# Kernel optimization log

Hardware: AMD Instinct MI355X
Metric: run time of the kernel (lower is better)

## Reference

```python
import jax, jax.numpy as jnp
import numpy as np

D_MODEL, D_STATE, D_CONV, D_INNER = 1024, 16, 4, 2048
B, S = 1, 2048
EPS = 1e-5


def setup_inputs() -> dict:
    key = jax.random.key(0)
    ks = jax.random.split(key, 8)
    sc = 0.02
    return {
        "x": jax.random.normal(ks[0], (B, S, D_MODEL), jnp.float32),
        "ln_g": jnp.ones((D_MODEL,), jnp.float32),
        "ln_b": jnp.zeros((D_MODEL,), jnp.float32),
        "in_w": jax.random.normal(ks[1], (2 * D_INNER, D_MODEL), jnp.float32) * sc,
        "conv_w": jax.random.normal(ks[2], (D_INNER, 1, D_CONV), jnp.float32) * sc,  # depthwise OIH
        "conv_b": jax.random.normal(ks[3], (D_INNER,), jnp.float32) * sc,
        "xproj_w": jax.random.normal(ks[4], (2 * D_STATE + 1, D_INNER), jnp.float32) * sc,
        "dt_w": jax.random.normal(ks[5], (D_INNER, 1), jnp.float32) * sc,
        "dt_b": jax.random.normal(ks[6], (D_INNER,), jnp.float32) * sc,
        "A_log": jnp.log(jnp.arange(1, D_STATE + 1, dtype=jnp.float32)),
        "D": jnp.ones((D_INNER,), jnp.float32),
        "out_w": jax.random.normal(ks[7], (D_MODEL, D_INNER), jnp.float32) * sc,
    }


def reference(x, ln_g, ln_b, in_w, conv_w, conv_b, xproj_w, dt_w, dt_b, A_log, D, out_w):
    b, s, _ = x.shape
    d_inner = D.shape[0]
    d_state = A_log.shape[0]
    d_conv = conv_w.shape[-1]
    residual = x

    # LayerNorm
    mu = jnp.mean(x, axis=-1, keepdims=True)
    var = jnp.mean(jnp.square(x - mu), axis=-1, keepdims=True)
    xn = (x - mu) * jax.lax.rsqrt(var + EPS) * ln_g + ln_b

    # in_proj, split into x and gate z
    xz = jnp.einsum('bsd,ed->bse', xn, in_w)  # [B,S,2*d_inner]
    xi, z = jnp.split(xz, 2, axis=-1)

    # causal depthwise conv1d (torch pads d_conv-1 both sides then crops to seq_len)
    xc = jnp.transpose(xi, (0, 2, 1))  # [B,C,S]
    xc = jnp.pad(xc, ((0, 0), (0, 0), (d_conv - 1, 0)))
    xc = jax.lax.conv_general_dilated(
        xc, conv_w, window_strides=(1,), padding='VALID',
        dimension_numbers=('NCH', 'OIH', 'NCH'), feature_group_count=d_inner)
    xc = xc + conv_b[None, :, None]
    xs = jax.nn.silu(jnp.transpose(xc, (0, 2, 1)))  # [B,S,d_inner]

    # SSM projections
    xp = jnp.einsum('bsd,ed->bse', xs, xproj_w)  # [B,S,2*d_state+1]
    delta = jax.nn.softplus(xp[..., :1] * dt_w[:, 0] + dt_b)  # [B,S,d_inner]
    Bm = xp[..., 1:1 + d_state]  # [B,S,N]
    Cm = xp[..., 1 + d_state:]   # [B,S,N]
    A = -jnp.exp(A_log)          # [N]

    dA = jnp.exp(delta[..., None] * A)                      # [B,S,d_inner,N]
    dBx = delta[..., None] * Bm[:, :, None, :] * xs[..., None]  # [B,S,d_inner,N]

    def step(h, inp):
        dA_t, dBx_t, C_t = inp
        h = dA_t * h + dBx_t                     # [B,d_inner,N]
        y_t = jnp.einsum('bdn,bn->bd', h, C_t)   # [B,d_inner]
        return h, y_t

    h0 = jnp.zeros((b, d_inner, d_state), x.dtype)
    _, ys = jax.lax.scan(step, h0, (jnp.moveaxis(dA, 1, 0),
                                    jnp.moveaxis(dBx, 1, 0),
                                    jnp.moveaxis(Cm, 1, 0)))
    y = jnp.moveaxis(ys, 0, 1) + xs * D  # [B,S,d_inner]

    y = y * jax.nn.silu(z)
    out = jnp.einsum('bse,de->bsd', y, out_w)
    return out + residual
```

## Files before the change

kernel.cpp:

```cpp
#include <hip/hip_runtime.h>
#include <cstdint>
#include <cstddef>

#define D_MODEL 1024
#define D_STATE 16
#define D_CONV  4
#define D_INNER 2048
#define SEQ     2048
#define NCHUNK  128
#define CLEN    16
#define NGRP    8
#define GCH     16
#define LN_EPS  1e-5f

typedef unsigned short ushort_t;
typedef __attribute__((ext_vector_type(8))) short short8;
typedef __attribute__((ext_vector_type(4))) float f32x4;

__device__ __forceinline__ ushort_t f2bf(float x) {
  union { float f; uint32_t u; } v; v.f = x;
  uint32_t r = (v.u + 0x7fffu + ((v.u >> 16) & 1u)) >> 16;
  return (ushort_t)r;
}
__device__ __forceinline__ float bf2f(ushort_t u) {
  union { uint32_t x; float f; } v; v.x = ((uint32_t)u) << 16; return v.f;
}

__device__ __forceinline__ void async16(void* lds, const void* g) {
  __builtin_amdgcn_global_load_lds(
      (const __attribute__((address_space(1))) unsigned int*)g,
      (__attribute__((address_space(3))) unsigned int*)lds, 16, 0, 0);
}

__device__ __forceinline__ float softplus_f(float x) {
  if (x > 20.f) return x;
  if (x < -20.f) return __expf(x);
  return __logf(1.f + __expf(x));
}

__device__ __forceinline__ void dapow(float g1, float* da) {
  float g2 = g1 * g1, g4 = g2 * g2, g8 = g4 * g4;
  #pragma unroll
  for (int n = 0; n < 16; n++) {
    int e = n + 1;
    float v = (e & 1) ? g1 : 1.f;
    if (e & 2) v *= g2;
    if (e & 4) v *= g4;
    if (e & 8) v *= g8;
    da[n] = v;
  }
}

__global__ __launch_bounds__(256) void prep_kernel(const float* __restrict__ x,
                                                   const float* __restrict__ g,
                                                   const float* __restrict__ b,
                                                   const float* __restrict__ inw,
                                                   const float* __restrict__ outw,
                                                   const float* __restrict__ xpw,
                                                   ushort_t* __restrict__ xn_bf,
                                                   ushort_t* __restrict__ inw_bf,
                                                   ushort_t* __restrict__ outw_bf,
                                                   ushort_t* __restrict__ xpw_bf) {
  int blk = blockIdx.x;
  if (blk < SEQ) {
    int row = blk;
    const float4* xr = (const float4*)(x + (size_t)row * D_MODEL);
    float4 v = xr[threadIdx.x];
    float s  = v.x + v.y + v.z + v.w;
    float ss = v.x * v.x + v.y * v.y + v.z * v.z + v.w * v.w;
    #pragma unroll
    for (int o = 32; o; o >>= 1) { s += __shfl_down(s, o); ss += __shfl_down(ss, o); }
    __shared__ float sbuf[8], ssbuf[8];
    int wid = threadIdx.x >> 6, lane = threadIdx.x & 63;
    if (lane == 0) { sbuf[wid] = s; ssbuf[wid] = ss; }
    __syncthreads();
    if (threadIdx.x == 0) {
      float t = 0.f, t2 = 0.f;
      for (int i = 0; i < 4; i++) { t += sbuf[i]; t2 += ssbuf[i]; }
      float mu = t / D_MODEL;
      sbuf[4] = mu;
      ssbuf[4] = rsqrtf(t2 / D_MODEL - mu * mu + LN_EPS);
    }
    __syncthreads();
    float mu = sbuf[4], inv = ssbuf[4];
    float4 gv = ((const float4*)g)[threadIdx.x];
    float4 bv = ((const float4*)b)[threadIdx.x];
    ushort_t o4[4];
    o4[0] = f2bf((v.x - mu) * inv * gv.x + bv.x);
    o4[1] = f2bf((v.y - mu) * inv * gv.y + bv.y);
    o4[2] = f2bf((v.z - mu) * inv * gv.z + bv.z);
    o4[3] = f2bf((v.w - mu) * inv * gv.w + bv.w);
    *(ushort4*)&xn_bf[(size_t)row * D_MODEL + threadIdx.x * 4] =
        make_ushort4(o4[0], o4[1], o4[2], o4[3]);
  } else {
    int idx = (blk - SEQ) * 256 + threadIdx.x;
    const int n1 = 2 * D_INNER * D_MODEL;
    const int n2 = D_MODEL * D_INNER;
    const int n3 = 64 * D_INNER;
    if (idx < n1) {
      inw_bf[idx] = f2bf(inw[idx]);
    } else if (idx < n1 + n2) {
      int j = idx - n1;
      outw_bf[j] = f2bf(outw[j]);
    } else if (idx < n1 + n2 + n3) {
      int j = idx - n1 - n2;
      xpw_bf[j] = (j < 33 * D_INNER) ? f2bf(xpw[j]) : (ushort_t)0;
    }
  }
}

template <int BM, int BN, int KDIM, int EPI, int NBUF, int KSPLIT>
__global__ __launch_bounds__(256, 2) void gemm_pipe(const ushort_t* __restrict__ A,
                                                    const ushort_t* __restrict__ B,
                                                    void* __restrict__ Cout,
                                                    const float* __restrict__ R,
                                                    int N) {
  constexpr int KT = KDIM / 32 / KSPLIT;
  constexpr int K2 = KDIM * 2;
  constexpr int IA = BM / 64, IB = BN / 64;
  constexpr int S  = IA + IB;
  constexpr int W  = (NBUF - 2) * S;
  constexpr int WTM = BM / 2, WTN = BN / 2;
  constexpr int MREP = WTM / 16, NREP = WTN / 16;
  __shared__ __align__(16) ushort_t As[NBUF][BM * 32];
  __shared__ __align__(16) ushort_t Bs[NBUF][BN * 32];

  const int nwg = gridDim.x * gridDim.y;
  int bid = blockIdx.y * gridDim.x + blockIdx.x;
  int swz = (bid & 7) * (nwg >> 3) + (bid >> 3);
  int bn = swz % gridDim.x, bm = swz / gridDim.x;
  int ks = 0;
  if constexpr (KSPLIT > 1) { ks = bn; bn = 0; }
  const int tid = threadIdx.x, wid = tid >> 6, lane = tid & 63;
  const int wm = wid >> 1, wn = wid & 1;
  const int row0A = bm * BM, row0B = bn * BN;
  const size_t kbase = (size_t)ks * KT * 64;

  const char* gA[IA];
  const char* gB[IB];
  #pragma unroll
  for (int i = 0; i < IA; i++) {
    int o = i * 4096 + tid * 16;
    int r = o >> 6, src = (o & 63) ^ ((r & 3) << 4);
    gA[i] = (const char*)A + (size_t)(row0A + r) * K2 + src + kbase;
  }
  #pragma unroll
  for (int i = 0; i < IB; i++) {
    int o = i * 4096 + tid * 16;
    int r = o >> 6, src = (o & 63) ^ ((r & 3) << 4);
    gB[i] = (const char*)B + (size_t)(row0B + r) * K2 + src + kbase;
  }
  const int ldsW = wid * 1024;

  auto STAGE = [&](int bb, int kt) {
    int kb = kt * 64;
    #pragma unroll
    for (int i = 0; i < IA; i++)
      async16((char*)&As[bb][0] + i * 4096 + ldsW, gA[i] + kb);
    #pragma unroll
    for (int i = 0; i < IB; i++)
      async16((char*)&Bs[bb][0] + i * 4096 + ldsW, gB[i] + kb);
  };

  #pragma unroll
  for (int p = 0; p < NBUF - 1; p++) STAGE(p, p);

  int offA[MREP], offB[NREP];
  #pragma unroll
  for (int m = 0; m < MREP; m++) {
    int row = wm * WTM + m * 16 + (lane & 15);
    offA[m] = row * 64 + ((((lane >> 4)) ^ (row & 3)) << 4);
  }
  #pragma unroll
  for (int n = 0; n < NREP; n++) {
    int row = wn * WTN + n * 16 + (lane & 15);
    offB[n] = row * 64 + ((((lane >> 4)) ^ (row & 3)) << 4);
  }

  f32x4 acc[MREP][NREP] = {};
  int cur = 0;
  for (int kt = 0; kt < KT; kt++) {
    if (kt < KT - 1) {
      if constexpr (W == 6)       asm volatile("s_waitcnt vmcnt(6)" ::: "memory");
      else if constexpr (W == 8)  asm volatile("s_waitcnt vmcnt(8)" ::: "memory");
      else if constexpr (W == 12) asm volatile("s_waitcnt vmcnt(12)" ::: "memory");
      else                        asm volatile("s_waitcnt vmcnt(0)" ::: "memory");
    } else {
      asm volatile("s_waitcnt vmcnt(0)" ::: "memory");
    }
    __builtin_amdgcn_s_barrier();
    __builtin_amdgcn_sched_barrier(0);
    const char* Ab = (const char*)&As[cur][0];
    const char* Bb = (const char*)&Bs[cur][0];
    short8 af[MREP], bf[NREP];
    #pragma unroll
    for (int m = 0; m < MREP; m++) af[m] = *(const short8*)(Ab + offA[m]);
    #pragma unroll
    for (int n = 0; n < NREP; n++) bf[n] = *(const short8*)(Bb + offB[n]);
    if (kt + NBUF - 1 < KT) {
      int b2 = cur + NBUF - 1; if (b2 >= NBUF) b2 -= NBUF;
      STAGE(b2, kt + NBUF - 1);
    }
    __builtin_amdgcn_s_setprio(1);
    #pragma unroll
    for (int m = 0; m < MREP; m++)
      #pragma unroll
      for (int n = 0; n < NREP; n++)
        acc[m][n] = __builtin_amdgcn_mfma_f32_16x16x32_bf16(af[m], bf[n], acc[m][n], 0, 0, 0);
    __builtin_amdgcn_s_setprio(0);
    cur++; if (cur == NBUF) cur = 0;
  }

  #pragma unroll
  for (int m = 0; m < MREP; m++)
    #pragma unroll
    for (int n = 0; n < NREP; n++) {
      int r0 = row0A + wm * WTM + m * 16 + ((lane >> 4) << 2);
      int c  = row0B + wn * WTN + n * 16 + (lane & 15);
      #pragma unroll
      for (int q = 0; q < 4; q++) {
        if constexpr (EPI == 0) {
          ((ushort_t*)Cout)[(size_t)(r0 + q) * N + c] = f2bf(acc[m][n][q]);
        } else if constexpr (EPI == 1) {
          size_t idx = (size_t)(r0 + q) * N + c;
          ((float*)Cout)[idx] = acc[m][n][q] + R[idx];
        } else {
          if (c < 33)
            ((float*)Cout)[((size_t)ks * SEQ + r0 + q) * 33 + c] = acc[m][n][q];
        }
      }
    }
}

__global__ __launch_bounds__(256) void conv_silu_kernel(const ushort_t* __restrict__ xz_bf,
                                                        const float* __restrict__ cw,
                                                        const float* __restrict__ cb,
                                                        ushort_t* __restrict__ xs_bf) {
  const int t = blockIdx.x;
  const int d0 = threadIdx.x * 8;
  short8 rows[4];
  #pragma unroll
  for (int k = 0; k < 4; k++) {
    int tt = t - 3 + k;
    if (tt >= 0) rows[k] = *(const short8*)&xz_bf[(size_t)tt * (2 * D_INNER) + d0];
    else         rows[k] = (short8)0;
  }
  short8 o8;
  #pragma unroll
  for (int j = 0; j < 8; j++) {
    float4 w = ((const float4*)cw)[d0 + j];
    float acc = cb[d0 + j]
              + bf2f((ushort_t)rows[0][j]) * w.x
              + bf2f((ushort_t)rows[1][j]) * w.y
              + bf2f((ushort_t)rows[2][j]) * w.z
              + bf2f((ushort_t)rows[3][j]) * w.w;
    float sg = 1.f / (1.f + __expf(-acc));
    o8[j] = (short)f2bf(acc * sg);
  }
  *(short8*)&xs_bf[(size_t)t * D_INNER + d0] = o8;
}

__global__ __launch_bounds__(256) void scan_pass1(const ushort_t* __restrict__ xs_bf,
                                                  const float* __restrict__ xpp,
                                                  const float* __restrict__ dt_w,
                                                  const float* __restrict__ dt_b,
                                                  const float* __restrict__ A_log,
                                                  float* __restrict__ Hp,
                                                  float* __restrict__ Sd) {
  int c = blockIdx.x;
  int d0 = blockIdx.y * 512 + threadIdx.x;
  __shared__ float Bsh[CLEN][16], drs[CLEN], Ash[16];
  {
    int t = threadIdx.x >> 4, n = threadIdx.x & 15;
    const size_t P = (size_t)SEQ * 33;
    size_t rb = (size_t)(c * CLEN + t) * 33;
    float sB = 0.f;
    #pragma unroll
    for (int k = 0; k < 8; k++) sB += xpp[k * P + rb + 1 + n];
    Bsh[t][n] = sB;
    if (threadIdx.x < CLEN) {
      size_t rr = (size_t)(c * CLEN + threadIdx.x) * 33;
      float sD = 0.f;
      #pragma unroll
      for (int k = 0; k < 8; k++) sD += xpp[k * P + rr];
      drs[threadIdx.x] = sD;
    } else if (threadIdx.x < CLEN + 16) {
      int n2 = threadIdx.x - CLEN;
      Ash[n2] = -__expf(A_log[n2]);
    }
  }
  __syncthreads();
  bool fastA = true;
  #pragma unroll
  for (int n = 0; n < 16; n++) fastA = fastA && (fabsf(Ash[n] + (float)(n + 1)) < 1e-4f * (n + 1));
  float dw[2] = {dt_w[d0], dt_w[d0 + 256]};
  float db[2] = {dt_b[d0], dt_b[d0 + 256]};
  float h[2][16] = {};
  float S[2] = {0.f, 0.f};
  size_t tb = (size_t)(c * CLEN) * D_INNER + d0;
  float xv[2] = {bf2f(xs_bf[tb]), bf2f(xs_bf[tb + 256])};
  for (int t = 0; t < CLEN; t++) {
    float nx[2] = {0.f, 0.f};
    if (t + 1 < CLEN) {
      nx[0] = bf2f(xs_bf[tb + D_INNER]);
      nx[1] = bf2f(xs_bf[tb + D_INNER + 256]);
    }
    float bb[16];
    *(float4*)&bb[0]  = *(const float4*)&Bsh[t][0];
    *(float4*)&bb[4]  = *(const float4*)&Bsh[t][4];
    *(float4*)&bb[8]  = *(const float4*)&Bsh[t][8];
    *(float4*)&bb[12] = *(const float4*)&Bsh[t][12];
    float drt = drs[t];
    #pragma unroll
    for (int u = 0; u < 2; u++) {
      float delta = softplus_f(drt * dw[u] + db[u]);
      S[u] += delta;
      float w = delta * xv[u];
      if (fastA) {
        float da[16];
        dapow(__expf(-delta), da);
        #pragma unroll
        for (int n = 0; n < 16; n++) h[u][n] = da[n] * h[u][n] + w * bb[n];
      } else {
        #pragma unroll
        for (int n = 0; n < 16; n++) h[u][n] = __expf(delta * Ash[n]) * h[u][n] + w * bb[n];
      }
    }
    xv[0] = nx[0]; xv[1] = nx[1];
    tb += D_INNER;
  }
  #pragma unroll
  for (int u = 0; u < 2; u++) {
    int d = d0 + u * 256;
    size_t base = ((size_t)c * D_INNER + d) * 16;
    #pragma unroll
    for (int n = 0; n < 16; n += 4)
      *(float4*)&Hp[base + n] = make_float4(h[u][n], h[u][n + 1], h[u][n + 2], h[u][n + 3]);
    Sd[(size_t)c * D_INNER + d] = S[u];
  }
}

__global__ __launch_bounds__(256) void combineA(const float* __restrict__ Hp,
                                                const float* __restrict__ Sd,
                                                const float* __restrict__ A_log,
                                                float* __restrict__ Hl,
                                                float* __restrict__ Slocp,
                                                float* __restrict__ Hgtot,
                                                float* __restrict__ Sgtot) {
  int g = blockIdx.x;
  int idx = blockIdx.y * 256 + threadIdx.x;
  int d = idx >> 4, n = idx & 15;
  float An = -__expf(A_log[n]);
  float h = 0.f, S = 0.f;
  const size_t stride = (size_t)D_INNER * 16;
  #pragma unroll 4
  for (int j = 0; j < GCH; j++) {
    int c = g * GCH + j;
    Hl[(size_t)c * stride + idx] = h;
    if (n == 0) Slocp[(size_t)c * D_INNER + d] = S;
    float Sc = Sd[(size_t)c * D_INNER + d];
    float hp = Hp[(size_t)c * stride + idx];
    h = __expf(An * Sc) * h + hp;
    S += Sc;
  }
  Hgtot[(size_t)g * stride + idx] = h;
  if (n == 0) Sgtot[(size_t)g * D_INNER + d] = S;
}

__global__ __launch_bounds__(256) void combineB(const float* __restrict__ Hgtot,
                                                const float* __restrict__ Sgtot,
                                                const float* __restrict__ A_log,
                                                float* __restrict__ Ginit) {
  int idx = blockIdx.x * 256 + threadIdx.x;
  int d = idx >> 4, n = idx & 15;
  float An = -__expf(A_log[n]);
  float G = 0.f;
  const size_t stride = (size_t)D_INNER * 16;
  #pragma unroll
  for (int g = 0; g < NGRP; g++) {
    Ginit[(size_t)g * stride + idx] = G;
    G = __expf(An * Sgtot[(size_t)g * D_INNER + d]) * G + Hgtot[(size_t)g * stride + idx];
  }
}

__global__ __launch_bounds__(256) void scan_pass2(const ushort_t* __restrict__ xs_bf,
                                                  const float* __restrict__ xpp,
                                                  const ushort_t* __restrict__ xz_bf,
                                                  const float* __restrict__ dt_w,
                                                  const float* __restrict__ dt_b,
                                                  const float* __restrict__ A_log,
                                                  const float* __restrict__ Dp,
                                                  const float* __restrict__ Hl,
                                                  const float* __restrict__ Slocp,
                                                  const float* __restrict__ Ginit,
                                                  ushort_t* __restrict__ y_bf) {
  int c = blockIdx.x;
  int d0 = blockIdx.y * 512 + threadIdx.x;
  __shared__ float Bsh[CLEN][16], Csh[CLEN][16], drs[CLEN], Ash[16];
  {
    int t = threadIdx.x >> 4, n = threadIdx.x & 15;
    const size_t P = (size_t)SEQ * 33;
    size_t rb = (size_t)(c * CLEN + t) * 33;
    float sB = 0.f, sC = 0.f;
    #pragma unroll
    for (int k = 0; k < 8; k++) {
      sB += xpp[k * P + rb + 1 + n];
      sC += xpp[k * P + rb + 17 + n];
    }
    Bsh[t][n] = sB;
    Csh[t][n] = sC;
    if (threadIdx.x < CLEN) {
      size_t rr = (size_t)(c * CLEN + threadIdx.x) * 33;
      float sD = 0.f;
      #pragma unroll
      for (int k = 0; k < 8; k++) sD += xpp[k * P + rr];
      drs[threadIdx.x] = sD;
    } else if (threadIdx.x < CLEN + 16) {
      int n2 = threadIdx.x - CLEN;
      Ash[n2] = -__expf(A_log[n2]);
    }
  }
  __syncthreads();
  bool fastA = true;
  #pragma unroll
  for (int n = 0; n < 16; n++) fastA = fastA && (fabsf(Ash[n] + (float)(n + 1)) < 1e-4f * (n + 1));
  float dw[2] = {dt_w[d0], dt_w[d0 + 256]};
  float db[2] = {dt_b[d0], dt_b[d0 + 256]};
  float Dd[2] = {Dp[d0], Dp[d0 + 256]};
  int g8 = c >> 4;
  float h[2][16];
  #pragma unroll
  for (int u = 0; u < 2; u++) {
    int d = d0 + u * 256;
    size_t hb = ((size_t)c * D_INNER + d) * 16;
    size_t gb = ((size_t)g8 * D_INNER + d) * 16;
    float Slp = Slocp[(size_t)c * D_INNER + d];
    float hl[16], gi[16];
    #pragma unroll
    for (int n = 0; n < 16; n += 4) {
      *(float4*)&hl[n] = *(const float4*)&Hl[hb + n];
      *(float4*)&gi[n] = *(const float4*)&Ginit[gb + n];
    }
    if (fastA) {
      float pw[16];
      dapow(__expf(-Slp), pw);
      #pragma unroll
      for (int n = 0; n < 16; n++) h[u][n] = hl[n] + pw[n] * gi[n];
    } else {
      #pragma unroll
      for (int n = 0; n < 16; n++) h[u][n] = hl[n] + __expf(Ash[n] * Slp) * gi[n];
    }
  }
  size_t tb = (size_t)(c * CLEN) * D_INNER + d0;
  size_t zb = (size_t)(c * CLEN) * (2 * D_INNER) + D_INNER + d0;
  float xv[2] = {bf2f(xs_bf[tb]), bf2f(xs_bf[tb + 256])};
  float zv[2] = {bf2f(xz_bf[zb]), bf2f(xz_bf[zb + 256])};
  for (int t = 0; t < CLEN; t++) {
    float nx[2] = {0.f, 0.f}, nz[2] = {0.f, 0.f};
    if (t + 1 < CLEN) {
      nx[0] = bf2f(xs_bf[tb + D_INNER]);
      nx[1] = bf2f(xs_bf[tb + D_INNER + 256]);
      nz[0] = bf2f(xz_bf[zb + 2 * D_INNER]);
      nz[1] = bf2f(xz_bf[zb + 2 * D_INNER + 256]);
    }
    float bb[16], cc[16];
    *(float4*)&bb[0]  = *(const float4*)&Bsh[t][0];
    *(float4*)&bb[4]  = *(const float4*)&Bsh[t][4];
    *(float4*)&bb[8]  = *(const float4*)&Bsh[t][8];
    *(float4*)&bb[12] = *(const float4*)&Bsh[t][12];
    *(float4*)&cc[0]  = *(const float4*)&Csh[t][0];
    *(float4*)&cc[4]  = *(const float4*)&Csh[t][4];
    *(float4*)&cc[8]  = *(const float4*)&Csh[t][8];
    *(float4*)&cc[12] = *(const float4*)&Csh[t][12];
    float drt = drs[t];
    size_t ti = (size_t)(c * CLEN + t);
    #pragma unroll
    for (int u = 0; u < 2; u++) {
      float delta = softplus_f(drt * dw[u] + db[u]);
      float w = delta * xv[u];
      float y = 0.f;
      if (fastA) {
        float da[16];
        dapow(__expf(-delta), da);
        #pragma unroll
        for (int n = 0; n < 16; n++) {
          h[u][n] = da[n] * h[u][n] + w * bb[n];
          y += h[u][n] * cc[n];
        }
      } else {
        #pragma unroll
        for (int n = 0; n < 16; n++) {
          h[u][n] = __expf(delta * Ash[n]) * h[u][n] + w * bb[n];
          y += h[u][n] * cc[n];
        }
      }
      float z = zv[u];
      float sz = z / (1.f + __expf(-z));
      float out = (y + xv[u] * Dd[u]) * sz;
      y_bf[ti * D_INNER + d0 + u * 256] = f2bf(out);
    }
    xv[0] = nx[0]; xv[1] = nx[1];
    zv[0] = nz[0]; zv[1] = nz[1];
    tb += D_INNER; zb += 2 * D_INNER;
  }
}

extern "C" void kernel_launch(void* const* d_in, const int* in_sizes, int n_in,
                              void* d_out, int out_size, void* d_ws, size_t ws_size,
                              hipStream_t stream) {
  const float* x      = (const float*)d_in[0];
  const float* ln_g   = (const float*)d_in[1];
  const float* ln_b   = (const float*)d_in[2];
  const float* in_w   = (const float*)d_in[3];
  const float* conv_w = (const float*)d_in[4];
  const float* conv_b = (const float*)d_in[5];
  const float* xproj_w= (const float*)d_in[6];
  const float* dt_w   = (const float*)d_in[7];
  const float* dt_b   = (const float*)d_in[8];
  const float* A_log  = (const float*)d_in[9];
  const float* Dp     = (const float*)d_in[10];
  const float* out_w  = (const float*)d_in[11];
  float* out = (float*)d_out;

  char* ws = (char*)d_ws;
  size_t off = 0;
  auto alloc = [&](size_t bytes) { char* p = ws + off; off += (bytes + 255) & ~(size_t)255; return p; };
  ushort_t* xz_bf   = (ushort_t*)alloc((size_t)SEQ * 2 * D_INNER * 2);
  ushort_t* xn_bf   = (ushort_t*)alloc((size_t)SEQ * D_MODEL * 2);
  ushort_t* inw_bf  = (ushort_t*)alloc((size_t)2 * D_INNER * D_MODEL * 2);
  ushort_t* outw_bf = (ushort_t*)alloc((size_t)D_MODEL * D_INNER * 2);
  ushort_t* xpw_bf  = (ushort_t*)alloc((size_t)64 * D_INNER * 2);
  ushort_t* xs_bf   = (ushort_t*)alloc((size_t)SEQ * D_INNER * 2);
  float*    xp_part = (float*)   alloc((size_t)8 * SEQ * 33 * 4);
  float*    Hp      = (float*)   alloc((size_t)NCHUNK * D_INNER * 16 * 4);
  float*    Hl      = (float*)   alloc((size_t)NCHUNK * D_INNER * 16 * 4);
  float*    Sd      = (float*)   alloc((size_t)NCHUNK * D_INNER * 4);
  float*    Slocp   = (float*)   alloc((size_t)NCHUNK * D_INNER * 4);
  float*    Hgtot   = (float*)   alloc((size_t)NGRP * D_INNER * 16 * 4);
  float*    Sgtot   = (float*)   alloc((size_t)NGRP * D_INNER * 4);
  float*    Ginit   = (float*)   alloc((size_t)NGRP * D_INNER * 16 * 4);
  ushort_t* y_bf    = (ushort_t*)alloc((size_t)SEQ * D_INNER * 2);
  (void)ws_size;

  const int ncvt = 2 * D_INNER * D_MODEL + D_MODEL * D_INNER + 64 * D_INNER;
  prep_kernel<<<SEQ + (ncvt + 255) / 256, 256, 0, stream>>>(
      x, ln_g, ln_b, in_w, out_w, xproj_w, xn_bf, inw_bf, outw_bf, xpw_bf);
  gemm_pipe<256, 128, D_MODEL, 0, 3, 1><<<dim3(2 * D_INNER / 128, SEQ / 256), 256, 0, stream>>>(
      xn_bf, inw_bf, xz_bf, nullptr, 2 * D_INNER);
  conv_silu_kernel<<<SEQ, 256, 0, stream>>>(xz_bf, conv_w, conv_b, xs_bf);
  gemm_pipe<64, 64, D_INNER, 3, 6, 8><<<dim3(8, SEQ / 64), 256, 0, stream>>>(
      xs_bf, xpw_bf, xp_part, nullptr, 64);
  scan_pass1<<<dim3(NCHUNK, D_INNER / 512), 256, 0, stream>>>(xs_bf, xp_part, dt_w, dt_b, A_log, Hp, Sd);
  combineA<<<dim3(NGRP, D_INNER * 16 / 256), 256, 0, stream>>>(Hp, Sd, A_log, Hl, Slocp, Hgtot, Sgtot);
  combineB<<<D_INNER * 16 / 256, 256, 0, stream>>>(Hgtot, Sgtot, A_log, Ginit);
  scan_pass2<<<dim3(NCHUNK, D_INNER / 512), 256, 0, stream>>>(xs_bf, xp_part, xz_bf, dt_w, dt_b, A_log,
                                                              Dp, Hl, Slocp, Ginit, y_bf);
  gemm_pipe<64, 64, D_INNER, 1, 6, 1><<<dim3(D_MODEL / 64, SEQ / 64), 256, 0, stream>>>(
      y_bf, outw_bf, out, x, D_MODEL);
}
```

Baseline: 135.4 us.

## Vectorize weight conversion, widen conv per-block, store scan states in bf16, retile in_proj

The weight-conversion part of the prep kernel now handles four elements per thread using float4 loads and ushort4 stores. The conv+SiLU kernel computes four timesteps per block from a shared 7-row window, so overlapping input rows and weights are loaded once instead of repeatedly. The chunked-scan intermediate states (Hp, Hl, Hgtot, Ginit) are stored in bf16 instead of fp32, halving their memory traffic at the cost of precision in the scan carry. The in_proj GEMM tile changes from 256x128 with 3 buffers to 128x128 with 4 buffers, doubling the number of blocks.

```diff
diff --git a/kernel.cpp b/kernel.cpp
--- a/kernel.cpp
+++ b/kernel.cpp
@@ -93,19 +93,23 @@
     *(ushort4*)&xn_bf[(size_t)row * D_MODEL + threadIdx.x * 4] =
         make_ushort4(o4[0], o4[1], o4[2], o4[3]);
   } else {
-    int idx = (blk - SEQ) * 256 + threadIdx.x;
+    int idx = ((blk - SEQ) * 256 + threadIdx.x) * 4;
     const int n1 = 2 * D_INNER * D_MODEL;
     const int n2 = D_MODEL * D_INNER;
     const int n3 = 64 * D_INNER;
-    if (idx < n1) {
-      inw_bf[idx] = f2bf(inw[idx]);
-    } else if (idx < n1 + n2) {
-      int j = idx - n1;
-      outw_bf[j] = f2bf(outw[j]);
-    } else if (idx < n1 + n2 + n3) {
-      int j = idx - n1 - n2;
-      xpw_bf[j] = (j < 33 * D_INNER) ? f2bf(xpw[j]) : (ushort_t)0;
-    }
+    const float* src; ushort_t* dst; int j;
+    if (idx < n1) { src = inw; dst = inw_bf; j = idx; }
+    else if (idx < n1 + n2) { src = outw; dst = outw_bf; j = idx - n1; }
+    else if (idx < n1 + n2 + n3) {
+      j = idx - n1 - n2;
+      if (j < 33 * D_INNER) { src = xpw; dst = xpw_bf; }
+      else {
+        *(ushort4*)&xpw_bf[j] = make_ushort4(0, 0, 0, 0);
+        return;
+      }
+    } else return;
+    float4 v = *(const float4*)&src[j];
+    *(ushort4*)&dst[j] = make_ushort4(f2bf(v.x), f2bf(v.y), f2bf(v.z), f2bf(v.w));
   }
 }
 
@@ -236,28 +240,34 @@
                                                         const float* __restrict__ cw,
                                                         const float* __restrict__ cb,
                                                         ushort_t* __restrict__ xs_bf) {
-  const int t = blockIdx.x;
+  const int t0 = blockIdx.x * 4;
   const int d0 = threadIdx.x * 8;
-  short8 rows[4];
-  #pragma unroll
-  for (int k = 0; k < 4; k++) {
-    int tt = t - 3 + k;
-    if (tt >= 0) rows[k] = *(const short8*)&xz_bf[(size_t)tt * (2 * D_INNER) + d0];
-    else         rows[k] = (short8)0;
-  }
-  short8 o8;
-  #pragma unroll
-  for (int j = 0; j < 8; j++) {
-    float4 w = ((const float4*)cw)[d0 + j];
-    float acc = cb[d0 + j]
-              + bf2f((ushort_t)rows[0][j]) * w.x
-              + bf2f((ushort_t)rows[1][j]) * w.y
-              + bf2f((ushort_t)rows[2][j]) * w.z
-              + bf2f((ushort_t)rows[3][j]) * w.w;
-    float sg = 1.f / (1.f + __expf(-acc));
-    o8[j] = (short)f2bf(acc * sg);
-  }
-  *(short8*)&xs_bf[(size_t)t * D_INNER + d0] = o8;
+  short8 win[7];
+  #pragma unroll
+  for (int j = 0; j < 7; j++) {
+    int tt = t0 - 3 + j;
+    if (tt >= 0) win[j] = *(const short8*)&xz_bf[(size_t)tt * (2 * D_INNER) + d0];
+    else         win[j] = (short8)0;
+  }
+  float4 w[8];
+  float  cbv[8];
+  #pragma unroll
+  for (int j = 0; j < 8; j++) { w[j] = ((const float4*)cw)[d0 + j]; cbv[j] = cb[d0 + j]; }
+  #pragma unroll
+  for (int q = 0; q < 4; q++) {
+    short8 o8;
+    #pragma unroll
+    for (int j = 0; j < 8; j++) {
+      float acc = cbv[j]
+                + bf2f((ushort_t)win[q][j])     * w[j].x
+                + bf2f((ushort_t)win[q + 1][j]) * w[j].y
+                + bf2f((ushort_t)win[q + 2][j]) * w[j].z
+                + bf2f((ushort_t)win[q + 3][j]) * w[j].w;
+      float sg = 1.f / (1.f + __expf(-acc));
+      o8[j] = (short)f2bf(acc * sg);
+    }
+    *(short8*)&xs_bf[(size_t)(t0 + q) * D_INNER + d0] = o8;
+  }
 }
 
 __global__ __launch_bounds__(256) void scan_pass1(const ushort_t* __restrict__ xs_bf,
@@ -265,7 +275,7 @@
                                                   const float* __restrict__ dt_w,
                                                   const float* __restrict__ dt_b,
                                                   const float* __restrict__ A_log,
-                                                  float* __restrict__ Hp,
+                                                  ushort_t* __restrict__ Hp,
                                                   float* __restrict__ Sd) {
   int c = blockIdx.x;
   int d0 = blockIdx.y * 512 + threadIdx.x;
@@ -333,19 +343,21 @@
   for (int u = 0; u < 2; u++) {
     int d = d0 + u * 256;
     size_t base = ((size_t)c * D_INNER + d) * 16;
-    #pragma unroll
-    for (int n = 0; n < 16; n += 4)
-      *(float4*)&Hp[base + n] = make_float4(h[u][n], h[u][n + 1], h[u][n + 2], h[u][n + 3]);
+    short8 p0, p1;
+    #pragma unroll
+    for (int n = 0; n < 8; n++) { p0[n] = (short)f2bf(h[u][n]); p1[n] = (short)f2bf(h[u][8 + n]); }
+    *(short8*)&Hp[base] = p0;
+    *(short8*)&Hp[base + 8] = p1;
     Sd[(size_t)c * D_INNER + d] = S[u];
   }
 }
 
-__global__ __launch_bounds__(256) void combineA(const float* __restrict__ Hp,
+__global__ __launch_bounds__(256) void combineA(const ushort_t* __restrict__ Hp,
                                                 const float* __restrict__ Sd,
                                                 const float* __restrict__ A_log,
-                                                float* __restrict__ Hl,
+                                                ushort_t* __restrict__ Hl,
                                                 float* __restrict__ Slocp,
-                                                float* __restrict__ Hgtot,
+                                                ushort_t* __restrict__ Hgtot,
                                                 float* __restrict__ Sgtot) {
   int g = blockIdx.x;
   int idx = blockIdx.y * 256 + threadIdx.x;
@@ -356,21 +368,21 @@
   #pragma unroll 4
   for (int j = 0; j < GCH; j++) {
     int c = g * GCH + j;
-    Hl[(size_t)c * stride + idx] = h;
+    Hl[(size_t)c * stride + idx] = f2bf(h);
     if (n == 0) Slocp[(size_t)c * D_INNER + d] = S;
     float Sc = Sd[(size_t)c * D_INNER + d];
-    float hp = Hp[(size_t)c * stride + idx];
+    float hp = bf2f(Hp[(size_t)c * stride + idx]);
     h = __expf(An * Sc) * h + hp;
     S += Sc;
   }
-  Hgtot[(size_t)g * stride + idx] = h;
+  Hgtot[(size_t)g * stride + idx] = f2bf(h);
   if (n == 0) Sgtot[(size_t)g * D_INNER + d] = S;
 }
 
-__global__ __launch_bounds__(256) void combineB(const float* __restrict__ Hgtot,
+__global__ __launch_bounds__(256) void combineB(const ushort_t* __restrict__ Hgtot,
                                                 const float* __restrict__ Sgtot,
                                                 const float* __restrict__ A_log,
-                                                float* __restrict__ Ginit) {
+                                                ushort_t* __restrict__ Ginit) {
   int idx = blockIdx.x * 256 + threadIdx.x;
   int d = idx >> 4, n = idx & 15;
   float An = -__expf(A_log[n]);
@@ -378,8 +390,8 @@
   const size_t stride = (size_t)D_INNER * 16;
   #pragma unroll
   for (int g = 0; g < NGRP; g++) {
-    Ginit[(size_t)g * stride + idx] = G;
-    G = __expf(An * Sgtot[(size_t)g * D_INNER + d]) * G + Hgtot[(size_t)g * stride + idx];
+    Ginit[(size_t)g * stride + idx] = f2bf(G);
+    G = __expf(An * Sgtot[(size_t)g * D_INNER + d]) * G + bf2f(Hgtot[(size_t)g * stride + idx]);
   }
 }
 
@@ -390,9 +402,9 @@
                                                   const float* __restrict__ dt_b,
                                                   const float* __restrict__ A_log,
                                                   const float* __restrict__ Dp,
-                                                  const float* __restrict__ Hl,
+                                                  const ushort_t* __restrict__ Hl,
                                                   const float* __restrict__ Slocp,
-                                                  const float* __restrict__ Ginit,
+                                                  const ushort_t* __restrict__ Ginit,
                                                   ushort_t* __restrict__ y_bf) {
   int c = blockIdx.x;
   int d0 = blockIdx.y * 512 + threadIdx.x;
@@ -435,11 +447,15 @@
     size_t hb = ((size_t)c * D_INNER + d) * 16;
     size_t gb = ((size_t)g8 * D_INNER + d) * 16;
     float Slp = Slocp[(size_t)c * D_INNER + d];
+    short8 hl0 = *(const short8*)&Hl[hb];
+    short8 hl1 = *(const short8*)&Hl[hb + 8];
+    short8 gi0 = *(const short8*)&Ginit[gb];
+    short8 gi1 = *(const short8*)&Ginit[gb + 8];
     float hl[16], gi[16];
     #pragma unroll
-    for (int n = 0; n < 16; n += 4) {
-      *(float4*)&hl[n] = *(const float4*)&Hl[hb + n];
-      *(float4*)&gi[n] = *(const float4*)&Ginit[gb + n];
+    for (int n = 0; n < 8; n++) {
+      hl[n] = bf2f((ushort_t)hl0[n]); hl[8 + n] = bf2f((ushort_t)hl1[n]);
+      gi[n] = bf2f((ushort_t)gi0[n]); gi[8 + n] = bf2f((ushort_t)gi1[n]);
     }
     if (fastA) {
       float pw[16];
@@ -532,22 +548,22 @@
   ushort_t* xpw_bf  = (ushort_t*)alloc((size_t)64 * D_INNER * 2);
   ushort_t* xs_bf   = (ushort_t*)alloc((size_t)SEQ * D_INNER * 2);
   float*    xp_part = (float*)   alloc((size_t)8 * SEQ * 33 * 4);
-  float*    Hp      = (float*)   alloc((size_t)NCHUNK * D_INNER * 16 * 4);
-  float*    Hl      = (float*)   alloc((size_t)NCHUNK * D_INNER * 16 * 4);
+  ushort_t* Hp      = (ushort_t*)alloc((size_t)NCHUNK * D_INNER * 16 * 2);
+  ushort_t* Hl      = (ushort_t*)alloc((size_t)NCHUNK * D_INNER * 16 * 2);
   float*    Sd      = (float*)   alloc((size_t)NCHUNK * D_INNER * 4);
   float*    Slocp   = (float*)   alloc((size_t)NCHUNK * D_INNER * 4);
-  float*    Hgtot   = (float*)   alloc((size_t)NGRP * D_INNER * 16 * 4);
+  ushort_t* Hgtot   = (ushort_t*)alloc((size_t)NGRP * D_INNER * 16 * 2);
   float*    Sgtot   = (float*)   alloc((size_t)NGRP * D_INNER * 4);
-  float*    Ginit   = (float*)   alloc((size_t)NGRP * D_INNER * 16 * 4);
+  ushort_t* Ginit   = (ushort_t*)alloc((size_t)NGRP * D_INNER * 16 * 2);
   ushort_t* y_bf    = (ushort_t*)alloc((size_t)SEQ * D_INNER * 2);
   (void)ws_size;
 
-  const int ncvt = 2 * D_INNER * D_MODEL + D_MODEL * D_INNER + 64 * D_INNER;
-  prep_kernel<<<SEQ + (ncvt + 255) / 256, 256, 0, stream>>>(
+  const int ncvt4 = (2 * D_INNER * D_MODEL + D_MODEL * D_INNER + 64 * D_INNER) / 4;
+  prep_kernel<<<SEQ + (ncvt4 + 255) / 256, 256, 0, stream>>>(
       x, ln_g, ln_b, in_w, out_w, xproj_w, xn_bf, inw_bf, outw_bf, xpw_bf);
-  gemm_pipe<256, 128, D_MODEL, 0, 3, 1><<<dim3(2 * D_INNER / 128, SEQ / 256), 256, 0, stream>>>(
+  gemm_pipe<128, 128, D_MODEL, 0, 4, 1><<<dim3(2 * D_INNER / 128, SEQ / 128), 256, 0, stream>>>(
       xn_bf, inw_bf, xz_bf, nullptr, 2 * D_INNER);
-  conv_silu_kernel<<<SEQ, 256, 0, stream>>>(xz_bf, conv_w, conv_b, xs_bf);
+  conv_silu_kernel<<<SEQ / 4, 256, 0, stream>>>(xz_bf, conv_w, conv_b, xs_bf);
   gemm_pipe<64, 64, D_INNER, 3, 6, 8><<<dim3(8, SEQ / 64), 256, 0, stream>>>(
       xs_bf, xpw_bf, xp_part, nullptr, 64);
   scan_pass1<<<dim3(NCHUNK, D_INNER / 512), 256, 0, stream>>>(xs_bf, xp_part, dt_w, dt_b, A_log, Hp, Sd);
```

New measurement: 118.7 us, median of 2. -12.4%, faster.
